# Kernel tuning notes

Hardware: AMD Instinct MI355X
Metric: run time of the kernel (lower is better)

## Reference

```python
import jax, jax.numpy as jnp
import numpy as np

EMBED = 768
NHEAD = 12
HEAD_DIM = EMBED // NHEAD


def setup_inputs() -> dict:
    key = jax.random.key(0)
    ks = jax.random.split(key, 6)
    bs, seq = 4, 2048
    x = jax.random.normal(ks[0], (bs, seq, EMBED), dtype=jnp.float32)
    attmask = jax.random.randint(ks[1], (bs, seq), 0, 2, dtype=jnp.int32)
    # xavier-uniform-ish init for weights
    lim_qkv = float(np.sqrt(6.0 / (EMBED + 3 * EMBED)))
    W_qkv = jax.random.uniform(ks[2], (EMBED, 3 * EMBED), minval=-lim_qkv, maxval=lim_qkv, dtype=jnp.float32)
    b_qkv = jnp.zeros((3 * EMBED,), dtype=jnp.float32)
    lim_p = float(np.sqrt(6.0 / (EMBED + EMBED)))
    W_proj = jax.random.uniform(ks[3], (EMBED, EMBED), minval=-lim_p, maxval=lim_p, dtype=jnp.float32)
    b_proj = jnp.zeros((EMBED,), dtype=jnp.float32)
    return {"x": x, "attmask": attmask, "W_qkv": W_qkv, "b_qkv": b_qkv, "W_proj": W_proj, "b_proj": b_proj}


def reference(x, attmask, W_qkv, b_qkv, W_proj, b_proj):
    bs, seq, embed = x.shape
    qkv = x @ W_qkv + b_qkv                     # [bs, seq, 3*embed]
    q, k, v = jnp.split(qkv, 3, axis=-1)
    def to_heads(t):
        return t.reshape(bs, seq, NHEAD, HEAD_DIM).transpose(0, 2, 1, 3)  # [bs, h, seq, d]
    q, k, v = to_heads(q), to_heads(k), to_heads(v)
    scale = 1.0 / np.sqrt(HEAD_DIM).astype(np.float32)
    scores = jnp.einsum('bhqd,bhkd->bhqk', q, k) * scale  # [bs, h, seq, seq]
    mask = (attmask == 0)[:, None, None, :]               # [bs,1,1,seq]
    scores = jnp.where(mask, jnp.asarray(-10000.0, scores.dtype), scores)
    att = jax.nn.softmax(scores, axis=-1)                  # dropout p=0.0 -> identity
    y = jnp.einsum('bhqk,bhkd->bhqd', att, v)              # [bs, h, seq, d]
    y = y.transpose(0, 2, 1, 3).reshape(bs, seq, embed)
    return y @ W_proj + b_proj
```

## Files before the change

### kernel.cpp

```cpp
#include <hip/hip_runtime.h>

typedef unsigned short u16;
typedef unsigned int u32;
typedef __attribute__((ext_vector_type(8))) short short8;
typedef __attribute__((ext_vector_type(4))) short s16x4;
typedef __attribute__((ext_vector_type(4))) float f32x4;

__device__ __forceinline__ float b2f(u16 u) {
    union { u32 i; float f; } v; v.i = ((u32)u) << 16; return v.f;
}
__device__ __forceinline__ u16 f2b(float f) {
    union { u32 i; float f; } v; v.f = f;
    u32 u = v.i;
    return (u16)((u + 0x7FFFu + ((u >> 16) & 1u)) >> 16);
}
__device__ __forceinline__ f32x4 zero4() {
    f32x4 v; v[0] = 0.f; v[1] = 0.f; v[2] = 0.f; v[3] = 0.f; return v;
}
__device__ __forceinline__ u32 cvtpk(float lo, float hi) {
    u32 d;
    asm("v_cvt_pk_bf16_f32 %0, %1, %2" : "=v"(d) : "v"(lo), "v"(hi));
    return d;
}
__device__ __forceinline__ float fexp2(float x) {
#if __has_builtin(__builtin_amdgcn_exp2f)
    return __builtin_amdgcn_exp2f(x);
#else
    return __expf(x * 0.6931471805599453f);
#endif
}
__device__ __forceinline__ void gload16(const u16* g, u16* l) {
    __builtin_amdgcn_global_load_lds(
        (const __attribute__((address_space(1))) u32*)g,
        (__attribute__((address_space(3))) u32*)l, 16, 0, 0);
}

__device__ __forceinline__ void tconv_body(const float* __restrict__ src,
                                           u16* __restrict__ dst,
                                           int K, int N, int bx, int by) {
    __shared__ u16 T[64][72];
    const int n0 = bx * 64, k0 = by * 64;
    const int tid = threadIdx.x;
    const int r = tid >> 3, cq = tid & 7;
#pragma unroll
    for (int half = 0; half < 2; half++) {
        const int k = k0 + half * 32 + r;
        const float* s = &src[(size_t)k * N + n0 + cq * 8];
        const float4 f0 = ((const float4*)s)[0];
        const float4 f1 = ((const float4*)s)[1];
        T[cq * 8 + 0][half * 32 + r] = f2b(f0.x);
        T[cq * 8 + 1][half * 32 + r] = f2b(f0.y);
        T[cq * 8 + 2][half * 32 + r] = f2b(f0.z);
        T[cq * 8 + 3][half * 32 + r] = f2b(f0.w);
        T[cq * 8 + 4][half * 32 + r] = f2b(f1.x);
        T[cq * 8 + 5][half * 32 + r] = f2b(f1.y);
        T[cq * 8 + 6][half * 32 + r] = f2b(f1.z);
        T[cq * 8 + 7][half * 32 + r] = f2b(f1.w);
    }
    __syncthreads();
#pragma unroll
    for (int half = 0; half < 2; half++) {
        const int n = half * 32 + r;
        short8 o = *(const short8*)&T[n][cq * 8];
        *(short8*)&dst[(size_t)(n0 + n) * K + k0 + cq * 8] = o;
    }
}

__global__ void prep_kernel(const float* __restrict__ x, u16* __restrict__ xb,
                            const float* __restrict__ Wqkv, u16* __restrict__ Wqkvb,
                            const float* __restrict__ Wproj, u16* __restrict__ Wprojb,
                            int n8x) {
    const int blk = blockIdx.x;
    if (blk < 432) {
        tconv_body(Wqkv, Wqkvb, 768, 2304, blk % 36, blk / 36);
    } else if (blk < 576) {
        const int id = blk - 432;
        tconv_body(Wproj, Wprojb, 768, 768, id % 12, id / 12);
    } else {
        const int stride = (1152 - 576) * 256;
        for (int i = (blk - 576) * 256 + threadIdx.x; i < n8x; i += stride) {
            const float* s = x + (size_t)i * 8;
            float4 a = ((const float4*)s)[0];
            float4 b = ((const float4*)s)[1];
            short8 o;
            o[0] = (short)f2b(a.x); o[1] = (short)f2b(a.y);
            o[2] = (short)f2b(a.z); o[3] = (short)f2b(a.w);
            o[4] = (short)f2b(b.x); o[5] = (short)f2b(b.y);
            o[6] = (short)f2b(b.z); o[7] = (short)f2b(b.w);
            ((short8*)xb)[i] = o;
        }
    }
}

template <int MODE>
__global__ __launch_bounds__(256, 2) void gemm_bt_kernel(
    const u16* __restrict__ A, const u16* __restrict__ Bt,
    const float* __restrict__ bias,
    u16* __restrict__ O0, u16* __restrict__ O1, u16* __restrict__ O2,
    float* __restrict__ Of,
    int M, int N, int K)
{
    __shared__ u16 As[128 * 64];
    __shared__ u16 Bs[128 * 64];

    const int tid = threadIdx.x;
    const int nwgx = gridDim.x;
    const int nwg = nwgx * gridDim.y;
    int lin = blockIdx.y * nwgx + blockIdx.x;
    lin = (lin & 7) * (nwg >> 3) + (lin >> 3);
    const int m0 = (lin / nwgx) * 128, n0 = (lin % nwgx) * 128;
    const int lane = tid & 63, w = tid >> 6;
    const int quad = lane >> 4, c = lane & 15;
    const int wm = (w & 1) * 64, wn = (w >> 1) * 64;

    f32x4 acc[4][4];
#pragma unroll
    for (int i = 0; i < 4; i++)
#pragma unroll
        for (int j = 0; j < 4; j++) acc[i][j] = zero4();

    const int srow = lane >> 3;
    const int scol = ((lane & 7) ^ ((srow & 1) << 2)) * 8;
    const size_t abase = (size_t)(m0 + w * 32 + srow) * K + scol;
    const size_t bbase = (size_t)(n0 + w * 32 + srow) * K + scol;
    u16* asl = &As[w * 32 * 64];
    u16* bsl = &Bs[w * 32 * 64];

    const int cpar = (c & 1) << 2;

    for (int k0 = 0; k0 < K; k0 += 64) {
        __syncthreads();
#pragma unroll
        for (int i = 0; i < 4; i++)
            gload16(A + abase + (size_t)(i * 8) * K + k0, asl + i * 512);
#pragma unroll
        for (int i = 0; i < 4; i++)
            gload16(Bt + bbase + (size_t)(i * 8) * K + k0, bsl + i * 512);
        asm volatile("s_waitcnt vmcnt(0)" ::: "memory");
        __syncthreads();

        short8 af[4][2], bfr[4][2];
#pragma unroll
        for (int mi = 0; mi < 4; mi++)
#pragma unroll
            for (int kk = 0; kk < 2; kk++)
                af[mi][kk] = *(const short8*)
                    &As[(wm + mi * 16 + c) * 64 + (((kk * 4 + quad) ^ cpar) * 8)];
#pragma unroll
        for (int ni = 0; ni < 4; ni++)
#pragma unroll
            for (int kk = 0; kk < 2; kk++)
                bfr[ni][kk] = *(const short8*)
                    &Bs[(wn + ni * 16 + c) * 64 + (((kk * 4 + quad) ^ cpar) * 8)];
#pragma unroll
        for (int kk = 0; kk < 2; kk++)
#pragma unroll
            for (int mi = 0; mi < 4; mi++)
#pragma unroll
                for (int ni = 0; ni < 4; ni++)
                    acc[mi][ni] = __builtin_amdgcn_mfma_f32_16x16x32_bf16(
                        af[mi][kk], bfr[ni][kk], acc[mi][ni], 0, 0, 0);
    }

#pragma unroll
    for (int ni = 0; ni < 4; ni++) {
        const int gc = n0 + wn + ni * 16 + c;
        const float bv = bias[gc];
        if (MODE == 0) {
            const int which = gc / 768;
            const int e = gc - which * 768;
            const int hh = e >> 6, d = e & 63;
            u16* op = (which == 0) ? O0 : (which == 1 ? O1 : O2);
#pragma unroll
            for (int mi = 0; mi < 4; mi++)
#pragma unroll
                for (int r = 0; r < 4; r++) {
                    const int gr = m0 + wm + mi * 16 + quad * 4 + r;
                    const int bb = gr >> 11, s = gr & 2047;
                    op[(((size_t)bb * 12 + hh) * 2048 + s) * 64 + d] =
                        f2b(acc[mi][ni][r] + bv);
                }
        } else {
#pragma unroll
            for (int mi = 0; mi < 4; mi++)
#pragma unroll
                for (int r = 0; r < 4; r++) {
                    const int gr = m0 + wm + mi * 16 + quad * 4 + r;
                    Of[(size_t)gr * N + gc] = acc[mi][ni][r] + bv;
                }
        }
    }
}

__global__ __launch_bounds__(256, 3) void attn_kernel(
    const u16* __restrict__ Q, const u16* __restrict__ Kv,
    const u16* __restrict__ Vv, const int* __restrict__ attmask,
    u16* __restrict__ Y)
{
    const int S = 2048, D = 64, NH = 12;
    __shared__ u16 Ks[64][72];
    __shared__ u16 Vs[64][68];
    __shared__ u16 Ps[4][2][16][72];
    __shared__ u16 msb[2048];

    const int tid = threadIdx.x;
    const int w = tid >> 6, lane = tid & 63;
    const int quad = lane >> 4, c = lane & 15;
    const int bh = blockIdx.x;
    const int qt = blockIdx.y;
    const int b = bh / NH, h = bh - b * NH;

    const u16* Qh = Q + (size_t)bh * S * D;
    const u16* Kh = Kv + (size_t)bh * S * D;
    const u16* Vh = Vv + (size_t)bh * S * D;
    const int q0 = qt * 128 + w * 16;

    short8 aq00 = *(const short8*)&Qh[(size_t)(q0 + c) * D + quad * 8];
    short8 aq01 = *(const short8*)&Qh[(size_t)(q0 + c) * D + 32 + quad * 8];
    short8 aq10 = *(const short8*)&Qh[(size_t)(q0 + 64 + c) * D + quad * 8];
    short8 aq11 = *(const short8*)&Qh[(size_t)(q0 + 64 + c) * D + 32 + quad * 8];

    for (int i = tid; i < S; i += 256)
        msb[i] = (attmask[b * S + i] == 0) ? (u16)0xC700 : (u16)0;

    f32x4 o_acc[2][4];
#pragma unroll
    for (int g = 0; g < 2; g++)
#pragma unroll
        for (int i = 0; i < 4; i++) o_acc[g][i] = zero4();
    float l0 = 0.f, l1 = 0.f;

    const int kpos = tid >> 2, kd = (tid & 3) * 8;
    const int p2 = tid >> 3, vd = (tid & 7) * 8;

    short8 k0r = *(const short8*)&Kh[(size_t)kpos * D + kd];
    short8 k1r = *(const short8*)&Kh[(size_t)kpos * D + kd + 32];
    short8 v0r = *(const short8*)&Vh[(size_t)(2 * p2) * D + vd];
    short8 v1r = *(const short8*)&Vh[(size_t)(2 * p2 + 1) * D + vd];

    const float SC = 0.18033688f;

    for (int kt = 0; kt < S / 64; kt++) {
        asm volatile("" ::: "memory");
        __builtin_amdgcn_s_barrier();
        asm volatile("" ::: "memory");
        *(short8*)&Ks[kpos][kd] = k0r;
        *(short8*)&Ks[kpos][kd + 32] = k1r;
#pragma unroll
        for (int j = 0; j < 8; j++) {
            u32 pk = (u32)(u16)v0r[j] | ((u32)(u16)v1r[j] << 16);
            *(u32*)&Vs[vd + j][2 * p2] = pk;
        }
        if (kt + 1 < S / 64) {
            const int nb = (kt + 1) * 64;
            k0r = *(const short8*)&Kh[(size_t)(nb + kpos) * D + kd];
            k1r = *(const short8*)&Kh[(size_t)(nb + kpos) * D + kd + 32];
            v0r = *(const short8*)&Vh[(size_t)(nb + 2 * p2) * D + vd];
            v1r = *(const short8*)&Vh[(size_t)(nb + 2 * p2 + 1) * D + vd];
        }
        asm volatile("s_waitcnt lgkmcnt(0)" ::: "memory");
        __builtin_amdgcn_s_barrier();
        asm volatile("" ::: "memory");

        const int kbase = kt * 64;

        f32x4 s0[4], s1[4];
#pragma unroll
        for (int ni = 0; ni < 4; ni++) { s0[ni] = zero4(); s1[ni] = zero4(); }
        __builtin_amdgcn_s_setprio(1);
#pragma unroll
        for (int ni = 0; ni < 4; ni++) {
            short8 bk0 = *(const short8*)&Ks[ni * 16 + c][quad * 8];
            short8 bk1 = *(const short8*)&Ks[ni * 16 + c][32 + quad * 8];
            s0[ni] = __builtin_amdgcn_mfma_f32_16x16x32_bf16(bk0, aq00, s0[ni], 0, 0, 0);
            s0[ni] = __builtin_amdgcn_mfma_f32_16x16x32_bf16(bk1, aq01, s0[ni], 0, 0, 0);
            s1[ni] = __builtin_amdgcn_mfma_f32_16x16x32_bf16(bk0, aq10, s1[ni], 0, 0, 0);
            s1[ni] = __builtin_amdgcn_mfma_f32_16x16x32_bf16(bk1, aq11, s1[ni], 0, 0, 0);
        }
        __builtin_amdgcn_s_setprio(0);

#pragma unroll
        for (int ni = 0; ni < 4; ni++) {
            const uint2 mb = *(const uint2*)&msb[kbase + ni * 16 + quad * 4];
            union { u32 i; float f; } e0, e1, e2, e3;
            e0.i = mb.x << 16; e1.i = mb.x & 0xffff0000u;
            e2.i = mb.y << 16; e3.i = mb.y & 0xffff0000u;
            {
                float p0 = fexp2(fmaf(s0[ni][0], SC, e0.f));
                float p1 = fexp2(fmaf(s0[ni][1], SC, e1.f));
                float p2f = fexp2(fmaf(s0[ni][2], SC, e2.f));
                float p3 = fexp2(fmaf(s0[ni][3], SC, e3.f));
                l0 += (p0 + p1) + (p2f + p3);
                uint2 pk;
                pk.x = cvtpk(p0, p1);
                pk.y = cvtpk(p2f, p3);
                *(uint2*)&Ps[w][0][c][ni * 16 + quad * 4] = pk;
            }
            {
                float p0 = fexp2(fmaf(s1[ni][0], SC, e0.f));
                float p1 = fexp2(fmaf(s1[ni][1], SC, e1.f));
                float p2f = fexp2(fmaf(s1[ni][2], SC, e2.f));
                float p3 = fexp2(fmaf(s1[ni][3], SC, e3.f));
                l1 += (p0 + p1) + (p2f + p3);
                uint2 pk;
                pk.x = cvtpk(p0, p1);
                pk.y = cvtpk(p2f, p3);
                *(uint2*)&Ps[w][1][c][ni * 16 + quad * 4] = pk;
            }
        }

        short8 ap00 = *(const short8*)&Ps[w][0][c][quad * 8];
        short8 ap01 = *(const short8*)&Ps[w][0][c][32 + quad * 8];
        short8 ap10 = *(const short8*)&Ps[w][1][c][quad * 8];
        short8 ap11 = *(const short8*)&Ps[w][1][c][32 + quad * 8];
        __builtin_amdgcn_s_setprio(1);
#pragma unroll
        for (int ni = 0; ni < 4; ni++) {
            union { short8 v8; s16x4 v4[2]; } u0, u1;
            u0.v4[0] = *(const s16x4*)&Vs[ni * 16 + c][quad * 8];
            u0.v4[1] = *(const s16x4*)&Vs[ni * 16 + c][quad * 8 + 4];
            u1.v4[0] = *(const s16x4*)&Vs[ni * 16 + c][32 + quad * 8];
            u1.v4[1] = *(const s16x4*)&Vs[ni * 16 + c][32 + quad * 8 + 4];
            o_acc[0][ni] = __builtin_amdgcn_mfma_f32_16x16x32_bf16(ap00, u0.v8, o_acc[0][ni], 0, 0, 0);
            o_acc[0][ni] = __builtin_amdgcn_mfma_f32_16x16x32_bf16(ap01, u1.v8, o_acc[0][ni], 0, 0, 0);
            o_acc[1][ni] = __builtin_amdgcn_mfma_f32_16x16x32_bf16(ap10, u0.v8, o_acc[1][ni], 0, 0, 0);
            o_acc[1][ni] = __builtin_amdgcn_mfma_f32_16x16x32_bf16(ap11, u1.v8, o_acc[1][ni], 0, 0, 0);
        }
        __builtin_amdgcn_s_setprio(0);
    }

    l0 += __shfl_xor(l0, 16);
    l0 += __shfl_xor(l0, 32);
    l1 += __shfl_xor(l1, 16);
    l1 += __shfl_xor(l1, 32);

    const size_t ybase = ((size_t)b * S) * 768 + h * 64;
#pragma unroll
    for (int r = 0; r < 4; r++) {
        const float lr0 = __shfl(l0, quad * 4 + r);
        const float lr1 = __shfl(l1, quad * 4 + r);
        const float inv0 = 1.f / fmaxf(lr0, 1e-30f);
        const float inv1 = 1.f / fmaxf(lr1, 1e-30f);
        const int srow0 = qt * 128 + w * 16 + quad * 4 + r;
        const int srow1 = srow0 + 64;
#pragma unroll
        for (int ni = 0; ni < 4; ni++) {
            Y[ybase + (size_t)srow0 * 768 + ni * 16 + c] = f2b(o_acc[0][ni][r] * inv0);
            Y[ybase + (size_t)srow1 * 768 + ni * 16 + c] = f2b(o_acc[1][ni][r] * inv1);
        }
    }
}

extern "C" void kernel_launch(void* const* d_in, const int* in_sizes, int n_in,
                              void* d_out, int out_size, void* d_ws, size_t ws_size,
                              hipStream_t stream) {
    const float* x     = (const float*)d_in[0];
    const int* attmask = (const int*)d_in[1];
    const float* Wqkv  = (const float*)d_in[2];
    const float* bqkv  = (const float*)d_in[3];
    const float* Wproj = (const float*)d_in[4];
    const float* bproj = (const float*)d_in[5];
    float* outf = (float*)d_out;

    u16* base = (u16*)d_ws;
    const size_t nx = 4ull * 2048 * 768;
    const size_t nwqkv = 768ull * 2304;
    const size_t nwproj = 768ull * 768;
    u16* xb     = base;
    u16* Wqkvb  = xb + nx;
    u16* Wprojb = Wqkvb + nwqkv;
    u16* Qb     = Wprojb + nwproj;
    const size_t headElems = 48ull * 2048 * 64;
    u16* Kb = Qb + headElems;
    u16* Vb = Kb + headElems;
    u16* Yb = Vb + headElems;

    prep_kernel<<<1152, 256, 0, stream>>>(x, xb, Wqkv, Wqkvb, Wproj, Wprojb,
                                          (int)(nx / 8));

    gemm_bt_kernel<0><<<dim3(18, 64), 256, 0, stream>>>(
        xb, Wqkvb, bqkv, Qb, Kb, Vb, nullptr, 8192, 2304, 768);
    attn_kernel<<<dim3(48, 16), 256, 0, stream>>>(Qb, Kb, Vb, attmask, Yb);
    gemm_bt_kernel<1><<<dim3(6, 64), 256, 0, stream>>>(
        Yb, Wprojb, bproj, nullptr, nullptr, nullptr, outf, 8192, 768, 768);
}
```

Before: 225.9 us.

## Double-buffer GEMM LDS tiles with BK=32 to overlap loads with MFMA

Restructures the shared GEMM kernel's K loop to use two LDS buffers of 128x32 tiles. The next tile's global-to-LDS loads are issued before computing the current tile, and a partial vmcnt wait replaces the full drain. This is meant to hide global load latency behind MFMA work. In exchange the K step is halved, doubling the barrier count per K, and the XOR swizzle is dropped, which may bring LDS bank conflicts on the fragment reads.

```diff
diff --git a/kernel.cpp b/kernel.cpp
--- a/kernel.cpp
+++ b/kernel.cpp
@@ -100,8 +100,8 @@
     float* __restrict__ Of,
     int M, int N, int K)
 {
-    __shared__ u16 As[128 * 64];
-    __shared__ u16 Bs[128 * 64];
+    __shared__ u16 As[2][128 * 32];
+    __shared__ u16 Bs[2][128 * 32];
 
     const int tid = threadIdx.x;
     const int nwgx = gridDim.x;
@@ -119,47 +119,55 @@
 #pragma unroll
         for (int j = 0; j < 4; j++) acc[i][j] = zero4();
 
-    const int srow = lane >> 3;
-    const int scol = ((lane & 7) ^ ((srow & 1) << 2)) * 8;
-    const size_t abase = (size_t)(m0 + w * 32 + srow) * K + scol;
-    const size_t bbase = (size_t)(n0 + w * 32 + srow) * K + scol;
-    u16* asl = &As[w * 32 * 64];
-    u16* bsl = &Bs[w * 32 * 64];
-
-    const int cpar = (c & 1) << 2;
-
-    for (int k0 = 0; k0 < K; k0 += 64) {
-        __syncthreads();
-#pragma unroll
-        for (int i = 0; i < 4; i++)
-            gload16(A + abase + (size_t)(i * 8) * K + k0, asl + i * 512);
-#pragma unroll
-        for (int i = 0; i < 4; i++)
-            gload16(Bt + bbase + (size_t)(i * 8) * K + k0, bsl + i * 512);
-        asm volatile("s_waitcnt vmcnt(0)" ::: "memory");
-        __syncthreads();
-
-        short8 af[4][2], bfr[4][2];
+    const int grow = w * 32 + (lane >> 2);
+    const int gcol = (lane & 3) * 8;
+    const size_t abase = (size_t)(m0 + grow) * K + gcol;
+    const size_t bbase = (size_t)(n0 + grow) * K + gcol;
+
+    {
+        u16* asl = &As[0][w * 1024];
+        u16* bsl = &Bs[0][w * 1024];
+        gload16(A + abase, asl);
+        gload16(A + abase + (size_t)16 * K, asl + 512);
+        gload16(Bt + bbase, bsl);
+        gload16(Bt + bbase + (size_t)16 * K, bsl + 512);
+    }
+
+    const int niter = K >> 5;
+    int cur = 0;
+    for (int it = 0; it < niter; it++) {
+        asm volatile("" ::: "memory");
+        __builtin_amdgcn_s_barrier();
+        asm volatile("" ::: "memory");
+        if (it + 1 < niter) {
+            const size_t k1 = (size_t)(it + 1) * 32;
+            u16* asl = &As[cur ^ 1][w * 1024];
+            u16* bsl = &Bs[cur ^ 1][w * 1024];
+            gload16(A + abase + k1, asl);
+            gload16(A + abase + (size_t)16 * K + k1, asl + 512);
+            gload16(Bt + bbase + k1, bsl);
+            gload16(Bt + bbase + (size_t)16 * K + k1, bsl + 512);
+            asm volatile("s_waitcnt vmcnt(4)" ::: "memory");
+        } else {
+            asm volatile("s_waitcnt vmcnt(0)" ::: "memory");
+        }
+        __builtin_amdgcn_s_barrier();
+        asm volatile("" ::: "memory");
+
+        short8 af[4], bfr[4];
 #pragma unroll
         for (int mi = 0; mi < 4; mi++)
-#pragma unroll
-            for (int kk = 0; kk < 2; kk++)
-                af[mi][kk] = *(const short8*)
-                    &As[(wm + mi * 16 + c) * 64 + (((kk * 4 + quad) ^ cpar) * 8)];
+            af[mi] = *(const short8*)&As[cur][(wm + mi * 16 + c) * 32 + quad * 8];
 #pragma unroll
         for (int ni = 0; ni < 4; ni++)
-#pragma unroll
-            for (int kk = 0; kk < 2; kk++)
-                bfr[ni][kk] = *(const short8*)
-                    &Bs[(wn + ni * 16 + c) * 64 + (((kk * 4 + quad) ^ cpar) * 8)];
-#pragma unroll
-        for (int kk = 0; kk < 2; kk++)
-#pragma unroll
-            for (int mi = 0; mi < 4; mi++)
-#pragma unroll
-                for (int ni = 0; ni < 4; ni++)
-                    acc[mi][ni] = __builtin_amdgcn_mfma_f32_16x16x32_bf16(
-                        af[mi][kk], bfr[ni][kk], acc[mi][ni], 0, 0, 0);
+            bfr[ni] = *(const short8*)&Bs[cur][(wn + ni * 16 + c) * 32 + quad * 8];
+#pragma unroll
+        for (int mi = 0; mi < 4; mi++)
+#pragma unroll
+            for (int ni = 0; ni < 4; ni++)
+                acc[mi][ni] = __builtin_amdgcn_mfma_f32_16x16x32_bf16(
+                    af[mi], bfr[ni], acc[mi][ni], 0, 0, 0);
+        cur ^= 1;
     }
 
 #pragma unroll
```

Measured after the change: 232.5 us. +2.9%, slower.
